# Performance work log

Hardware: AMD Instinct MI355X
Metric: run time of the kernel (lower is better)

## Reference

```python
import jax, jax.numpy as jnp
import numpy as np

B, S, D = 2, 1024, 1024
H, KV, HD = 16, 4, 64
E, F = 8, 3584
EPS = 1e-5
TOP_K = 2


def setup_inputs() -> dict:
    key = jax.random.key(0)
    ks = jax.random.split(key, 12)
    sc = 0.02
    inv_freq = 1.0 / (10000.0 ** (np.arange(0, HD, 2, dtype=np.float32) / HD))
    freqs = np.outer(np.arange(S, dtype=np.float32), inv_freq)
    emb = np.concatenate([freqs, freqs], axis=-1)  # [S, HD]
    return {
        'x': jax.random.normal(ks[0], (B, S, D), jnp.float32),
        'ln1_w': jnp.ones((D,), jnp.float32),
        'ln2_w': jnp.ones((D,), jnp.float32),
        'wq': jax.random.normal(ks[1], (H * HD, D), jnp.float32) * sc,
        'wk': jax.random.normal(ks[2], (KV * HD, D), jnp.float32) * sc,
        'wv': jax.random.normal(ks[3], (KV * HD, D), jnp.float32) * sc,
        'wo': jax.random.normal(ks[4], (D, H * HD), jnp.float32) * sc,
        'gate_w': jax.random.normal(ks[5], (E, D), jnp.float32) * sc,
        'w1': jax.random.normal(ks[6], (E, F, D), jnp.float32) * sc,
        'w2': jax.random.normal(ks[7], (E, D, F), jnp.float32) * sc,
        'w3': jax.random.normal(ks[8], (E, F, D), jnp.float32) * sc,
        'cos': jnp.asarray(np.cos(emb)),
        'sin': jnp.asarray(np.sin(emb)),
    }


def _rms_norm(x, w):
    var = jnp.mean(jnp.square(x), axis=-1, keepdims=True)
    return x * jax.lax.rsqrt(var + EPS) * w


def _rotate_half(x):
    x1, x2 = jnp.split(x, 2, axis=-1)
    return jnp.concatenate([-x2, x1], axis=-1)


def _attn(h, wq, wk, wv, wo, cos, sin):
    # h: [B,S,D]
    q = (h @ wq.T).reshape(B, S, H, HD).transpose(0, 2, 1, 3)      # [B,H,S,HD]
    k = (h @ wk.T).reshape(B, S, KV, HD).transpose(0, 2, 1, 3)     # [B,KV,S,HD]
    v = (h @ wv.T).reshape(B, S, KV, HD).transpose(0, 2, 1, 3)
    c = cos[None, None, :S, :]
    s = sin[None, None, :S, :]
    q = q * c + _rotate_half(q) * s
    k = k * c + _rotate_half(k) * s
    k = jnp.repeat(k, H // KV, axis=1)  # GQA expand -> [B,H,S,HD]
    v = jnp.repeat(v, H // KV, axis=1)
    scores = jnp.einsum('bhqd,bhkd->bhqk', q, k) / jnp.sqrt(jnp.float32(HD))
    causal = jnp.tril(jnp.ones((S, S), bool))
    scores = jnp.where(causal[None, None], scores, jnp.float32(-1e30))
    probs = jax.nn.softmax(scores, axis=-1)
    out = jnp.einsum('bhqk,bhkd->bhqd', probs, v)
    out = out.transpose(0, 2, 1, 3).reshape(B, S, H * HD)
    return out @ wo.T


def _moe(h, gate_w, w1, w2, w3):
    T = B * S
    hs = h.reshape(T, D)
    probs = jax.nn.softmax(hs @ gate_w.T, axis=-1)       # [T,E]
    _, sel = jax.lax.top_k(probs, TOP_K)                  # [T,2]
    rw = jnp.take_along_axis(probs, sel, axis=-1)
    rw = rw / jnp.sum(rw, axis=-1, keepdims=True)
    cw = jnp.zeros((T, E), hs.dtype).at[jnp.arange(T)[:, None], sel].add(rw)  # [T,E] combine weights
    h1 = jnp.einsum('td,efd->tef', hs, w1)               # [T,E,F]
    h3 = jnp.einsum('td,efd->tef', hs, w3)
    inter = jax.nn.silu(h1) * h3
    out = jnp.einsum('tef,edf,te->td', inter, w2, cw)
    return out.reshape(B, S, D)


def reference(x, ln1_w, ln2_w, wq, wk, wv, wo, gate_w, w1, w2, w3, cos, sin):
    h = x + _attn(_rms_norm(x, ln1_w), wq, wk, wv, wo, cos, sin)
    h = h + _moe(_rms_norm(h, ln2_w), gate_w, w1, w2, w3)
    return h
```

## Files before the change

kernel.cpp:

```cpp
#include <hip/hip_runtime.h>

typedef unsigned short u16;
using short8 = __attribute__((ext_vector_type(8))) short;
using f32x4  = __attribute__((ext_vector_type(4))) float;

#define TQ   2048
#define DM   1024
#define SLEN 1024
#define FDIM 3584
#define NEXP 8

static __device__ __forceinline__ u16 f2bf(float f) {
  union { float f; unsigned u; } a; a.f = f;
  unsigned r = a.u + 0x7fffu + ((a.u >> 16) & 1u);
  return (u16)(r >> 16);
}
static __device__ __forceinline__ float bf2f(u16 u) {
  union { unsigned u; float f; } a; a.u = ((unsigned)u) << 16;
  return a.f;
}
static __device__ __forceinline__ unsigned cvtpk(float lo, float hi) {
  unsigned r;
  asm volatile("v_cvt_pk_bf16_f32 %0, %1, %2" : "=v"(r) : "v"(lo), "v"(hi));
  return r;
}

static __device__ __forceinline__ void gload16(const void* g, void* l) {
  __builtin_amdgcn_global_load_lds((const __attribute__((address_space(1))) void*)g,
                                   (__attribute__((address_space(3))) void*)l, 16, 0, 0);
}

static __device__ __forceinline__ int xcd_lid(int bid, int cpx) {
  return (bid & 7) * cpx + (bid >> 3);
}

static __device__ __forceinline__ void cvtwr8(float4 a, float4 b, u16* dst) {
  uint4 u;
  u.x = cvtpk(a.x, a.y); u.y = cvtpk(a.z, a.w);
  u.z = cvtpk(b.x, b.y); u.w = cvtpk(b.z, b.w);
  *(uint4*)dst = u;
}

__global__ __launch_bounds__(256) void rmsnorm_kernel(
    const float* __restrict__ x, const float* __restrict__ w,
    u16* __restrict__ oh, u16* __restrict__ ol, float* __restrict__ of) {
  int t = blockIdx.x, tid = threadIdx.x;
  const float4* xr = (const float4*)(x + (size_t)t * DM);
  float4 v = xr[tid];
  float ss = v.x * v.x + v.y * v.y + v.z * v.z + v.w * v.w;
#pragma unroll
  for (int m = 1; m < 64; m <<= 1) ss += __shfl_xor(ss, m);
  __shared__ float red[4];
  if ((tid & 63) == 0) red[tid >> 6] = ss;
  __syncthreads();
  float tot = red[0] + red[1] + red[2] + red[3];
  float sc = rsqrtf(tot * (1.0f / DM) + 1e-5f);
  float4 wv = ((const float4*)w)[tid];
  float o0 = v.x * sc * wv.x, o1 = v.y * sc * wv.y, o2 = v.z * sc * wv.z, o3 = v.w * sc * wv.w;
  ushort4 hh;
  hh.x = f2bf(o0); hh.y = f2bf(o1); hh.z = f2bf(o2); hh.w = f2bf(o3);
  *(ushort4*)(oh + (size_t)t * DM + tid * 4) = hh;
  if (ol) {
    ushort4 ll;
    ll.x = f2bf(o0 - bf2f(hh.x)); ll.y = f2bf(o1 - bf2f(hh.y));
    ll.z = f2bf(o2 - bf2f(hh.z)); ll.w = f2bf(o3 - bf2f(hh.w));
    *(ushort4*)(ol + (size_t)t * DM + tid * 4) = ll;
  }
  if (of) {
    float4 o4; o4.x = o0; o4.y = o1; o4.z = o2; o4.w = o3;
    ((float4*)(of + (size_t)t * DM))[tid] = o4;
  }
}

__global__ __launch_bounds__(256) void wconv_split_kernel(
    const float* __restrict__ wq, const float* __restrict__ wk,
    const float* __restrict__ wv, const float* __restrict__ wo,
    u16* __restrict__ qkvh, u16* __restrict__ qkvl,
    u16* __restrict__ woh, u16* __restrict__ wol) {
  for (int i = blockIdx.x * 256 + threadIdx.x; i < 655360; i += 640 * 256) {
    int el = i * 4;
    const float* src; u16 *dh, *dl;
    if (el < 1572864) {
      int r = el >> 10, c = el & 1023;
      if (r < 1024) src = wq + el;
      else if (r < 1280) src = wk + (r - 1024) * 1024 + c;
      else src = wv + (r - 1280) * 1024 + c;
      dh = qkvh + el; dl = qkvl + el;
    } else {
      int e2 = el - 1572864;
      src = wo + e2; dh = woh + e2; dl = wol + e2;
    }
    float4 v = *(const float4*)src;
    ushort4 h, l;
    h.x = f2bf(v.x); h.y = f2bf(v.y); h.z = f2bf(v.z); h.w = f2bf(v.w);
    l.x = f2bf(v.x - bf2f(h.x)); l.y = f2bf(v.y - bf2f(h.y));
    l.z = f2bf(v.z - bf2f(h.z)); l.w = f2bf(v.w - bf2f(h.w));
    *(ushort4*)dh = h; *(ushort4*)dl = l;
  }
}

template <bool RESID>
__global__ __launch_bounds__(256) void gemm_split2_kernel(
    const u16* __restrict__ Ah, const u16* __restrict__ Al,
    const u16* __restrict__ Wh, const u16* __restrict__ Wl,
    float* __restrict__ C, const float* __restrict__ resid, int N, int cpx) {
  __shared__ u16 sAh[2][128][32], sAl[2][128][32], sWh[2][64][32], sWl[2][64][32];
  int lid = xcd_lid(blockIdx.x, cpx);
  int bm = lid & 15, bn = lid >> 4;
  int tid = threadIdx.x, lane = tid & 63, w = tid >> 6;
  int wm = w >> 1, wn = w & 1;
  int qi = lane & 15, g = lane >> 4;
  int lr = lane >> 2, lc = (lane & 3) * 8;
  const u16* pa0 = Ah + (size_t)(bm * 128 + w * 16 + lr) * DM + lc;
  const u16* pa1 = pa0 + 64 * DM;
  const u16* pl0 = Al + (size_t)(bm * 128 + w * 16 + lr) * DM + lc;
  const u16* pl1 = pl0 + 64 * DM;
  const u16* pw  = Wh + (size_t)(bn * 64 + w * 16 + lr) * DM + lc;
  const u16* pwl = Wl + (size_t)(bn * 64 + w * 16 + lr) * DM + lc;
  f32x4 acc[4][2] = {};
#define STG2(buf, kk) do { \
    gload16(pa0 + (kk), &sAh[buf][w * 16][0]); \
    gload16(pa1 + (kk), &sAh[buf][64 + w * 16][0]); \
    gload16(pl0 + (kk), &sAl[buf][w * 16][0]); \
    gload16(pl1 + (kk), &sAl[buf][64 + w * 16][0]); \
    gload16(pw  + (kk), &sWh[buf][w * 16][0]); \
    gload16(pwl + (kk), &sWl[buf][w * 16][0]); } while (0)
  STG2(0, 0);
  asm volatile("s_waitcnt vmcnt(0)" ::: "memory");
  __syncthreads();
  for (int ks = 0; ks < 32; ks++) {
    int cur = ks & 1;
    if (ks < 31) STG2(cur ^ 1, (ks + 1) * 32);
    short8 afh[4], afl[4], bfh[2], bfl[2];
#pragma unroll
    for (int i = 0; i < 4; i++) {
      afh[i] = *(short8*)&sAh[cur][wm * 64 + i * 16 + qi][g * 8];
      afl[i] = *(short8*)&sAl[cur][wm * 64 + i * 16 + qi][g * 8];
    }
#pragma unroll
    for (int i = 0; i < 2; i++) {
      bfh[i] = *(short8*)&sWh[cur][wn * 32 + i * 16 + qi][g * 8];
      bfl[i] = *(short8*)&sWl[cur][wn * 32 + i * 16 + qi][g * 8];
    }
#pragma unroll
    for (int mi = 0; mi < 4; mi++)
#pragma unroll
      for (int ni = 0; ni < 2; ni++) {
        f32x4 a = acc[mi][ni];
        a = __builtin_amdgcn_mfma_f32_16x16x32_bf16(afh[mi], bfh[ni], a, 0, 0, 0);
        a = __builtin_amdgcn_mfma_f32_16x16x32_bf16(afl[mi], bfh[ni], a, 0, 0, 0);
        a = __builtin_amdgcn_mfma_f32_16x16x32_bf16(afh[mi], bfl[ni], a, 0, 0, 0);
        acc[mi][ni] = a;
      }
    asm volatile("s_waitcnt vmcnt(0)" ::: "memory");
    __syncthreads();
  }
#undef STG2
#pragma unroll
  for (int mi = 0; mi < 4; mi++)
#pragma unroll
    for (int ni = 0; ni < 2; ni++) {
      int col = bn * 64 + wn * 32 + ni * 16 + qi;
#pragma unroll
      for (int r = 0; r < 4; r++) {
        int row = bm * 128 + wm * 64 + mi * 16 + g * 4 + r;
        float val = acc[mi][ni][r];
        if (RESID) val += resid[(size_t)row * N + col];
        C[(size_t)row * N + col] = val;
      }
    }
}

__global__ __launch_bounds__(256) void rope_split_kernel(
    const float* __restrict__ qkvf,
    const float* __restrict__ cosT, const float* __restrict__ sinT,
    u16* __restrict__ qh, u16* __restrict__ ql, u16* __restrict__ kh, u16* __restrict__ kl,
    u16* __restrict__ vh, u16* __restrict__ vl) {
  int t = blockIdx.x, tid = threadIdx.x;
  int s = t & (SLEN - 1);
  const float* rowp = qkvf + (size_t)t * 1536;
#pragma unroll
  for (int it = 0; it < 2; it++) {
    int i = it * 256 + tid;
    int hh = i >> 5, d = i & 31;
    float c = cosT[s * 64 + d], sn = sinT[s * 64 + d];
    size_t dst = (size_t)t * DM + hh * 64 + d;
    float x1 = rowp[hh * 64 + d], x2 = rowp[hh * 64 + d + 32];
    float o1 = x1 * c - x2 * sn;
    float o2 = x2 * c + x1 * sn;
    u16 h1 = f2bf(o1), h2 = f2bf(o2);
    qh[dst] = h1; qh[dst + 32] = h2;
    ql[dst] = f2bf(o1 - bf2f(h1)); ql[dst + 32] = f2bf(o2 - bf2f(h2));
  }
  if (tid < 128) {
    int hh = tid >> 5, d = tid & 31;
    float c = cosT[s * 64 + d], sn = sinT[s * 64 + d];
    size_t dst = (size_t)t * 256 + hh * 64 + d;
    float x1 = rowp[1024 + hh * 64 + d], x2 = rowp[1024 + hh * 64 + d + 32];
    float o1 = x1 * c - x2 * sn;
    float o2 = x2 * c + x1 * sn;
    u16 h1 = f2bf(o1), h2 = f2bf(o2);
    kh[dst] = h1; kh[dst + 32] = h2;
    kl[dst] = f2bf(o1 - bf2f(h1)); kl[dst + 32] = f2bf(o2 - bf2f(h2));
  }
  {
    size_t dst = (size_t)t * 256 + tid;
    float v = rowp[1280 + tid];
    u16 h = f2bf(v);
    vh[dst] = h; vl[dst] = f2bf(v - bf2f(h));
  }
}

__global__ __launch_bounds__(256) void attn_kernel(
    const u16* __restrict__ qh, const u16* __restrict__ ql,
    const u16* __restrict__ kh, const u16* __restrict__ kl,
    const u16* __restrict__ vh, const u16* __restrict__ vl,
    u16* __restrict__ oh, u16* __restrict__ ol) {
  __shared__ u16 sKh[64][72], sKl[64][72];
  __shared__ u16 sVh[64][72], sVl[64][72];
  __shared__ u16 sPh[4][16][72], sPl[4][16][72];
  int idx = blockIdx.x & 255;
  int p = idx & 7;
  int bh = idx >> 3;
  int b = bh >> 4, h = bh & 15, kvh = h >> 2;
  int qt = (blockIdx.x < 256) ? p : (15 - p);
  int tid = threadIdx.x, lane = tid & 63, w = tid >> 6;
  int qi = lane & 15, g = lane >> 4;
  int qrow = qt * 64 + w * 16 + qi;
  size_t qbase = ((size_t)(b * SLEN + qrow)) * DM + h * 64;
  short8 qfh[2], qfl[2];
#pragma unroll
  for (int ds = 0; ds < 2; ds++) {
    qfh[ds] = *(const short8*)(qh + qbase + ds * 32 + g * 8);
    qfl[ds] = *(const short8*)(ql + qbase + ds * 32 + g * 8);
  }
  f32x4 oacc[4] = {};
  float mrun = -1e30f, lrun = 0.f;
  int ktiles = qt + 1;
  for (int kt = 0; kt < ktiles; kt++) {
    __syncthreads();
    {
      int r = tid >> 3, cs = (tid & 7) * 8;
#pragma unroll
      for (int rr = 0; rr < 64; rr += 32) {
        int key = kt * 64 + rr + r;
        size_t src = ((size_t)(b * SLEN + key)) * 256 + kvh * 64 + cs;
        *(short8*)&sKh[rr + r][cs] = *(const short8*)(kh + src);
        *(short8*)&sKl[rr + r][cs] = *(const short8*)(kl + src);
        short8 vv = *(const short8*)(vh + src);
        short8 vv2 = *(const short8*)(vl + src);
#pragma unroll
        for (int j = 0; j < 8; j++) {
          sVh[cs + j][rr + r] = (u16)vv[j];
          sVl[cs + j][rr + r] = (u16)vv2[j];
        }
      }
    }
    __syncthreads();
    f32x4 sa[4];
#pragma unroll
    for (int kf = 0; kf < 4; kf++) {
      f32x4 a = {};
#pragma unroll
      for (int ds = 0; ds < 2; ds++) {
        short8 kfh = *(short8*)&sKh[kf * 16 + qi][ds * 32 + g * 8];
        short8 kfl = *(short8*)&sKl[kf * 16 + qi][ds * 32 + g * 8];
        a = __builtin_amdgcn_mfma_f32_16x16x32_bf16(kfh, qfh[ds], a, 0, 0, 0);
        a = __builtin_amdgcn_mfma_f32_16x16x32_bf16(kfl, qfh[ds], a, 0, 0, 0);
        a = __builtin_amdgcn_mfma_f32_16x16x32_bf16(kfh, qfl[ds], a, 0, 0, 0);
      }
      sa[kf] = a;
    }
    int qg = qt * 64 + w * 16 + qi;
    float sv[4][4];
    float tmax = -1e30f;
#pragma unroll
    for (int kf = 0; kf < 4; kf++)
#pragma unroll
      for (int r = 0; r < 4; r++) {
        int key = kt * 64 + kf * 16 + g * 4 + r;
        float s = sa[kf][r] * 0.125f;
        s = (key <= qg) ? s : -1e30f;
        sv[kf][r] = s;
        tmax = fmaxf(tmax, s);
      }
    tmax = fmaxf(tmax, __shfl_xor(tmax, 16));
    tmax = fmaxf(tmax, __shfl_xor(tmax, 32));
    float mn = fmaxf(mrun, tmax);
    float alpha = expf(mrun - mn);
    float psum = 0.f;
#pragma unroll
    for (int kf = 0; kf < 4; kf++) {
      float p0 = expf(sv[kf][0] - mn), p1 = expf(sv[kf][1] - mn);
      float p2 = expf(sv[kf][2] - mn), p3 = expf(sv[kf][3] - mn);
      psum += p0 + p1 + p2 + p3;
      ushort4 ph, pl;
      ph.x = f2bf(p0); ph.y = f2bf(p1); ph.z = f2bf(p2); ph.w = f2bf(p3);
      pl.x = f2bf(p0 - bf2f(ph.x)); pl.y = f2bf(p1 - bf2f(ph.y));
      pl.z = f2bf(p2 - bf2f(ph.z)); pl.w = f2bf(p3 - bf2f(ph.w));
      *(ushort4*)&sPh[w][qi][kf * 16 + g * 4] = ph;
      *(ushort4*)&sPl[w][qi][kf * 16 + g * 4] = pl;
    }
    psum += __shfl_xor(psum, 16);
    psum += __shfl_xor(psum, 32);
    lrun = lrun * alpha + psum;
    mrun = mn;
#pragma unroll
    for (int df = 0; df < 4; df++) {
      oacc[df][0] *= alpha; oacc[df][1] *= alpha;
      oacc[df][2] *= alpha; oacc[df][3] *= alpha;
    }
#pragma unroll
    for (int ks = 0; ks < 2; ks++) {
      short8 pfh = *(short8*)&sPh[w][qi][ks * 32 + g * 8];
      short8 pfl = *(short8*)&sPl[w][qi][ks * 32 + g * 8];
#pragma unroll
      for (int df = 0; df < 4; df++) {
        short8 vfh = *(short8*)&sVh[df * 16 + qi][ks * 32 + g * 8];
        short8 vfl = *(short8*)&sVl[df * 16 + qi][ks * 32 + g * 8];
        f32x4 a = oacc[df];
        a = __builtin_amdgcn_mfma_f32_16x16x32_bf16(vfh, pfh, a, 0, 0, 0);
        a = __builtin_amdgcn_mfma_f32_16x16x32_bf16(vfl, pfh, a, 0, 0, 0);
        a = __builtin_amdgcn_mfma_f32_16x16x32_bf16(vfh, pfl, a, 0, 0, 0);
        oacc[df] = a;
      }
    }
  }
  float inv = 1.0f / lrun;
  size_t obase = ((size_t)(b * SLEN + qt * 64 + w * 16 + qi)) * DM + h * 64;
#pragma unroll
  for (int df = 0; df < 4; df++) {
    float o0 = oacc[df][0] * inv, o1 = oacc[df][1] * inv;
    float o2 = oacc[df][2] * inv, o3 = oacc[df][3] * inv;
    ushort4 hh, ll;
    hh.x = f2bf(o0); hh.y = f2bf(o1); hh.z = f2bf(o2); hh.w = f2bf(o3);
    ll.x = f2bf(o0 - bf2f(hh.x)); ll.y = f2bf(o1 - bf2f(hh.y));
    ll.z = f2bf(o2 - bf2f(hh.z)); ll.w = f2bf(o3 - bf2f(hh.w));
    *(ushort4*)(oh + obase + df * 16 + g * 4) = hh;
    *(ushort4*)(ol + obase + df * 16 + g * 4) = ll;
  }
}

__global__ void zero8_kernel(int* p) { if (threadIdx.x < 8) p[threadIdx.x] = 0; }

__global__ __launch_bounds__(64) void gate_kernel(
    const float* __restrict__ hf, const float* __restrict__ gw,
    int* cnt, int* tok_e, int* tok_pos, float* tok_w) {
  int t = blockIdx.x, lane = threadIdx.x;
  float acc[8] = {0, 0, 0, 0, 0, 0, 0, 0};
  for (int i = lane; i < DM; i += 64) {
    float h = hf[(size_t)t * DM + i];
#pragma unroll
    for (int e = 0; e < 8; e++) acc[e] += h * gw[e * DM + i];
  }
#pragma unroll
  for (int e = 0; e < 8; e++)
#pragma unroll
    for (int m = 1; m < 64; m <<= 1) acc[e] += __shfl_xor(acc[e], m);
  if (lane == 0) {
    int i0 = 0;
#pragma unroll
    for (int e = 1; e < 8; e++) if (acc[e] > acc[i0]) i0 = e;
    int i1 = -1;
#pragma unroll
    for (int e = 0; e < 8; e++) if (e != i0 && (i1 < 0 || acc[e] > acc[i1])) i1 = e;
    float w0 = 1.0f;
    float w1 = expf(acc[i1] - acc[i0]);
    float rs = 1.0f / (w0 + w1);
    int p0 = atomicAdd(&cnt[i0], 1);
    int p1 = atomicAdd(&cnt[i1], 1);
    tok_e[t * 2] = i0; tok_e[t * 2 + 1] = i1;
    tok_pos[t * 2] = p0; tok_pos[t * 2 + 1] = p1;
    tok_w[t * 2] = w0 * rs; tok_w[t * 2 + 1] = w1 * rs;
  }
}

__global__ void schedule_kernel(const int* cnt, int* offs, int* mt,
                                int* row_e, int* row_bm) {
  if (threadIdx.x == 0) {
    int s = 0, m = 0;
    for (int e = 0; e < 8; e++) {
      offs[e] = s;
      int nb = (cnt[e] + 127) >> 7;
      for (int i = 0; i < nb; i++) { row_e[m] = e; row_bm[m] = i; m++; }
      s += cnt[e];
    }
    *mt = m;
  }
}

__global__ __launch_bounds__(256) void gather_kernel(
    const u16* __restrict__ hn2b, const int* __restrict__ tok_e,
    const int* __restrict__ tok_pos, const float* __restrict__ tok_w,
    const int* __restrict__ offs, u16* __restrict__ Xg,
    int* __restrict__ pair_tok, int* __restrict__ pair_slot, float* __restrict__ pair_w) {
  int t = blockIdx.x;
#pragma unroll
  for (int slot = 0; slot < 2; slot++) {
    int e = tok_e[t * 2 + slot];
    int p = offs[e] + tok_pos[t * 2 + slot];
    ((ushort4*)(Xg + (size_t)p * DM))[threadIdx.x] =
        ((const ushort4*)(hn2b + (size_t)t * DM))[threadIdx.x];
    if (threadIdx.x == 0) {
      pair_tok[p] = t; pair_slot[p] = slot; pair_w[p] = tok_w[t * 2 + slot];
    }
  }
}

__global__ __launch_bounds__(256) void moe_gemm13_kernel(
    const u16* __restrict__ Xg, const float* __restrict__ w1,
    const float* __restrict__ w3, const int* __restrict__ cnt,
    const int* __restrict__ offs, const int* __restrict__ mt,
    const int* __restrict__ row_e, const int* __restrict__ row_bm,
    u16* __restrict__ inter) {
  __shared__ u16 sA[3][128][32];
  __shared__ u16 sW1[3][64][32], sW3[3][64][32];
  int MT = *mt;
  int active = MT * 56;
  int cpx = (active + 7) >> 3;
  int xg8 = blockIdx.x >> 3;
  if (xg8 >= cpx) return;
  int lid = (blockIdx.x & 7) * cpx + xg8;
  if (lid >= active) return;
  int mrow = lid % MT, bn = lid / MT;
  int e = row_e[mrow], bm = row_bm[mrow];
  int count = cnt[e], off = offs[e];
  const u16* A = Xg + (size_t)off * DM;
  const float* W1 = w1 + (size_t)e * FDIM * DM;
  const float* W3 = w3 + (size_t)e * FDIM * DM;
  int tid = threadIdx.x, lane = tid & 63, w = tid >> 6;
  int wm = w >> 1, wn = w & 1;
  int qi = lane & 15, g = lane >> 4;
  int lrA = lane >> 2, lcA = (lane & 3) * 8;
  int ga0 = bm * 128 + w * 32 + lrA;      if (ga0 >= count) ga0 = count - 1;
  int ga1 = bm * 128 + w * 32 + 16 + lrA; if (ga1 >= count) ga1 = count - 1;
  const u16* pa0 = A + (size_t)ga0 * DM + lcA;
  const u16* pa1 = A + (size_t)ga1 * DM + lcA;
  int r16 = lane >> 2;
  int rW = w * 16 + r16;
  int cW = (lane & 3) * 8;
  const float* q1 = W1 + (size_t)(bn * 64 + rW) * DM + cW;
  const float* q3 = W3 + (size_t)(bn * 64 + rW) * DM + cW;
  int uW = ((lane & 3) ^ (r16 & 3)) * 8;
  f32x4 acc1[4][2] = {}, acc3[4][2] = {};
  float4 p1a = *(const float4*)q1, p1b = *(const float4*)(q1 + 4);
  float4 p3a = *(const float4*)q3, p3b = *(const float4*)(q3 + 4);
  float4 v1a = *(const float4*)(q1 + 32), v1b = *(const float4*)(q1 + 36);
  float4 v3a = *(const float4*)(q3 + 32), v3b = *(const float4*)(q3 + 36);
  __builtin_amdgcn_sched_barrier(0);
  gload16(pa0, &sA[0][w * 32][0]);
  gload16(pa1, &sA[0][w * 32 + 16][0]);
  gload16(pa0 + 32, &sA[1][w * 32][0]);
  gload16(pa1 + 32, &sA[1][w * 32 + 16][0]);
  asm volatile("s_waitcnt vmcnt(8)" ::: "memory");
  cvtwr8(p1a, p1b, &sW1[0][rW][uW]);
  cvtwr8(p3a, p3b, &sW3[0][rW][uW]);
  for (int ks = 0; ks < 32; ks++) {
    int cur = ks % 3;
    if (ks == 0)       asm volatile("s_waitcnt vmcnt(2) lgkmcnt(0)" ::: "memory");
    else if (ks == 31) asm volatile("s_waitcnt vmcnt(0) lgkmcnt(0)" ::: "memory");
    else               asm volatile("s_waitcnt vmcnt(6) lgkmcnt(0)" ::: "memory");
    __builtin_amdgcn_s_barrier();
    short8 af[4], b1[2], b3[2];
#pragma unroll
    for (int i = 0; i < 4; i++)
      af[i] = *(short8*)&sA[cur][wm * 64 + i * 16 + qi][g * 8];
#pragma unroll
    for (int ni = 0; ni < 2; ni++) {
      int rt = wn * 32 + ni * 16 + qi;
      int ui = (g ^ (rt & 3)) * 8;
      b1[ni] = *(short8*)&sW1[cur][rt][ui];
      b3[ni] = *(short8*)&sW3[cur][rt][ui];
    }
    __builtin_amdgcn_s_setprio(1);
#pragma unroll
    for (int mi = 0; mi < 4; mi++)
#pragma unroll
      for (int ni = 0; ni < 2; ni++) {
        acc1[mi][ni] = __builtin_amdgcn_mfma_f32_16x16x32_bf16(af[mi], b1[ni], acc1[mi][ni], 0, 0, 0);
        acc3[mi][ni] = __builtin_amdgcn_mfma_f32_16x16x32_bf16(af[mi], b3[ni], acc3[mi][ni], 0, 0, 0);
      }
    __builtin_amdgcn_s_setprio(0);
    if (ks < 31) {
      int nb = (ks + 1) % 3;
      cvtwr8(v1a, v1b, &sW1[nb][rW][uW]);
      cvtwr8(v3a, v3b, &sW3[nb][rW][uW]);
      if (ks < 30) {
        int k2 = (ks + 2) * 32;
        v1a = *(const float4*)(q1 + k2); v1b = *(const float4*)(q1 + k2 + 4);
        v3a = *(const float4*)(q3 + k2); v3b = *(const float4*)(q3 + k2 + 4);
        __builtin_amdgcn_sched_barrier(0);
        int ab = (ks + 2) % 3;
        gload16(pa0 + k2, &sA[ab][w * 32][0]);
        gload16(pa1 + k2, &sA[ab][w * 32 + 16][0]);
      }
    }
  }
#pragma unroll
  for (int mi = 0; mi < 4; mi++)
#pragma unroll
    for (int r = 0; r < 4; r++) {
      int row = bm * 128 + wm * 64 + mi * 16 + g * 4 + r;
      if (row < count) {
        size_t obase = (size_t)(off + row) * FDIM + bn * 64 + wn * 32;
#pragma unroll
        for (int ni = 0; ni < 2; ni++) {
          float c1 = acc1[mi][ni][r], c3 = acc3[mi][ni][r];
          float sv = c1 / (1.0f + expf(-c1)) * c3;
          inter[obase + ni * 16 + qi] = f2bf(sv);
        }
      }
    }
}

__global__ __launch_bounds__(256) void moe_gemm2_kernel(
    const u16* __restrict__ inter, const float* __restrict__ w2,
    const int* __restrict__ cnt, const int* __restrict__ offs,
    const int* __restrict__ mt, const int* __restrict__ row_e,
    const int* __restrict__ row_bm,
    const int* __restrict__ pair_tok, const int* __restrict__ pair_slot,
    const float* __restrict__ pair_w, float* __restrict__ pout) {
  __shared__ u16 sA[3][128][32];
  __shared__ u16 sW[3][64][32];
  int MT = *mt;
  int active = MT * 16;
  int cpx = (active + 7) >> 3;
  int xg8 = blockIdx.x >> 3;
  if (xg8 >= cpx) return;
  int lid = (blockIdx.x & 7) * cpx + xg8;
  if (lid >= active) return;
  int mrow = lid % MT, bn = lid / MT;
  int e = row_e[mrow], bm = row_bm[mrow];
  int count = cnt[e], off = offs[e];
  const u16* A = inter + (size_t)off * FDIM;
  const float* W = w2 + (size_t)e * DM * FDIM;
  int tid = threadIdx.x, lane = tid & 63, w = tid >> 6;
  int wm = w >> 1, wn = w & 1;
  int qi = lane & 15, g = lane >> 4;
  int lrA = lane >> 2, lcA = (lane & 3) * 8;
  int ga0 = bm * 128 + w * 32 + lrA;      if (ga0 >= count) ga0 = count - 1;
  int ga1 = bm * 128 + w * 32 + 16 + lrA; if (ga1 >= count) ga1 = count - 1;
  const u16* pa0 = A + (size_t)ga0 * FDIM + lcA;
  const u16* pa1 = A + (size_t)ga1 * FDIM + lcA;
  int r16 = lane >> 2;
  int rW = w * 16 + r16;
  int cW = (lane & 3) * 8;
  const float* qw = W + (size_t)(bn * 64 + rW) * FDIM + cW;
  int uW = ((lane & 3) ^ (r16 & 3)) * 8;
  f32x4 acc[4][2] = {};
  const int NK = FDIM / 32;
  float4 ta = *(const float4*)qw, tb = *(const float4*)(qw + 4);
  float4 va = *(const float4*)(qw + 32), vb = *(const float4*)(qw + 36);
  __builtin_amdgcn_sched_barrier(0);
  gload16(pa0, &sA[0][w * 32][0]);
  gload16(pa1, &sA[0][w * 32 + 16][0]);
  gload16(pa0 + 32, &sA[1][w * 32][0]);
  gload16(pa1 + 32, &sA[1][w * 32 + 16][0]);
  asm volatile("s_waitcnt vmcnt(6)" ::: "memory");
  cvtwr8(ta, tb, &sW[0][rW][uW]);
  for (int ks = 0; ks < NK; ks++) {
    int cur = ks % 3;
    if (ks == 0)           asm volatile("s_waitcnt vmcnt(2) lgkmcnt(0)" ::: "memory");
    else if (ks == NK - 1) asm volatile("s_waitcnt vmcnt(0) lgkmcnt(0)" ::: "memory");
    else                   asm volatile("s_waitcnt vmcnt(4) lgkmcnt(0)" ::: "memory");
    __builtin_amdgcn_s_barrier();
    short8 af[4], bfr[2];
#pragma unroll
    for (int i = 0; i < 4; i++)
      af[i] = *(short8*)&sA[cur][wm * 64 + i * 16 + qi][g * 8];
#pragma unroll
    for (int ni = 0; ni < 2; ni++) {
      int rt = wn * 32 + ni * 16 + qi;
      bfr[ni] = *(short8*)&sW[cur][rt][(g ^ (rt & 3)) * 8];
    }
    __builtin_amdgcn_s_setprio(1);
#pragma unroll
    for (int mi = 0; mi < 4; mi++)
#pragma unroll
      for (int ni = 0; ni < 2; ni++)
        acc[mi][ni] = __builtin_amdgcn_mfma_f32_16x16x32_bf16(af[mi], bfr[ni], acc[mi][ni], 0, 0, 0);
    __builtin_amdgcn_s_setprio(0);
    if (ks < NK - 1) {
      int nb = (ks + 1) % 3;
      cvtwr8(va, vb, &sW[nb][rW][uW]);
      if (ks < NK - 2) {
        int k2 = (ks + 2) * 32;
        va = *(const float4*)(qw + k2); vb = *(const float4*)(qw + k2 + 4);
        __builtin_amdgcn_sched_barrier(0);
        int ab = (ks + 2) % 3;
        gload16(pa0 + k2, &sA[ab][w * 32][0]);
        gload16(pa1 + k2, &sA[ab][w * 32 + 16][0]);
      }
    }
  }
#pragma unroll
  for (int mi = 0; mi < 4; mi++)
#pragma unroll
    for (int r = 0; r < 4; r++) {
      int row = bm * 128 + wm * 64 + mi * 16 + g * 4 + r;
      if (row < count) {
        int p = off + row;
        int t = pair_tok[p];
        float wgt = pair_w[p];
        size_t obase = ((size_t)pair_slot[p] * TQ + t) * DM + bn * 64 + wn * 32;
#pragma unroll
        for (int ni = 0; ni < 2; ni++)
          pout[obase + ni * 16 + qi] = acc[mi][ni][r] * wgt;
      }
    }
}

__global__ __launch_bounds__(256) void combine_kernel(
    const float* __restrict__ h, const float* __restrict__ pout, float* __restrict__ out) {
  size_t i = (size_t)blockIdx.x * 256 + threadIdx.x;
  float4 a = ((const float4*)h)[i];
  float4 b0 = ((const float4*)pout)[i];
  float4 b1 = ((const float4*)pout)[i + (size_t)TQ * DM / 4];
  float4 r;
  r.x = a.x + b0.x + b1.x; r.y = a.y + b0.y + b1.y;
  r.z = a.z + b0.z + b1.z; r.w = a.w + b0.w + b1.w;
  ((float4*)out)[i] = r;
}

extern "C" void kernel_launch(void* const* d_in, const int* in_sizes, int n_in,
                              void* d_out, int out_size, void* d_ws, size_t ws_size,
                              hipStream_t stream) {
  (void)in_sizes; (void)n_in; (void)out_size; (void)ws_size;
  const float* x    = (const float*)d_in[0];
  const float* ln1  = (const float*)d_in[1];
  const float* ln2  = (const float*)d_in[2];
  const float* wq   = (const float*)d_in[3];
  const float* wk   = (const float*)d_in[4];
  const float* wv   = (const float*)d_in[5];
  const float* wo   = (const float*)d_in[6];
  const float* gw   = (const float*)d_in[7];
  const float* w1   = (const float*)d_in[8];
  const float* w2   = (const float*)d_in[9];
  const float* w3   = (const float*)d_in[10];
  const float* cosT = (const float*)d_in[11];
  const float* sinT = (const float*)d_in[12];

  char* mb = (char*)d_ws;
  const size_t MB = 1024 * 1024;
  u16*   qhb  = (u16*)(mb + 0 * MB);
  u16*   qlb  = (u16*)(mb + 4 * MB);
  u16*   khb  = (u16*)(mb + 8 * MB);
  u16*   klb  = (u16*)(mb + 9 * MB);
  u16*   vhb  = (u16*)(mb + 10 * MB);
  u16*   vlb  = (u16*)(mb + 11 * MB);
  u16*   hn2b = (u16*)(mb + 0 * MB);
  float* hn2f = (float*)(mb + 4 * MB);
  u16*   ahb  = (u16*)(mb + 12 * MB);
  u16*   alb  = (u16*)(mb + 16 * MB);
  u16*   Xg   = (u16*)(mb + 12 * MB);
  u16*   hn1h = (u16*)(mb + 20 * MB);
  u16*   hn1l = (u16*)(mb + 24 * MB);
  u16*   inter= (u16*)(mb + 20 * MB);
  float* qkvf = (float*)(mb + 28 * MB);
  float* h_res= (float*)(mb + 48 * MB);
  u16*   woh  = (u16*)(mb + 56 * MB);
  u16*   wol  = (u16*)(mb + 58 * MB);
  float* pout = (float*)(mb + 56 * MB);
  u16*   wqkvh= (u16*)(mb + 60 * MB);
  u16*   wqkvl= (u16*)(mb + 63 * MB);
  int*   cnt  = (int*)(mb + 72 * MB);
  int*   offs = cnt + 8;
  int*   mtp  = cnt + 16;
  int*   row_e  = cnt + 17;
  int*   row_bm = cnt + 57;
  int*   tok_e  = cnt + 128;
  int*   tok_pos = tok_e + 4096;
  float* tok_w   = (float*)(tok_pos + 4096);
  int*   pair_tok  = (int*)(tok_w + 4096);
  int*   pair_slot = pair_tok + 4096;
  float* pair_w    = (float*)(pair_slot + 4096);

  wconv_split_kernel<<<640, 256, 0, stream>>>(wq, wk, wv, wo, wqkvh, wqkvl, woh, wol);
  rmsnorm_kernel<<<TQ, 256, 0, stream>>>(x, ln1, hn1h, hn1l, nullptr);
  gemm_split2_kernel<false><<<384, 256, 0, stream>>>(hn1h, hn1l, wqkvh, wqkvl, qkvf, nullptr, 1536, 48);
  rope_split_kernel<<<TQ, 256, 0, stream>>>(qkvf, cosT, sinT, qhb, qlb, khb, klb, vhb, vlb);
  attn_kernel<<<512, 256, 0, stream>>>(qhb, qlb, khb, klb, vhb, vlb, ahb, alb);
  gemm_split2_kernel<true><<<256, 256, 0, stream>>>(ahb, alb, woh, wol, h_res, x, 1024, 32);
  rmsnorm_kernel<<<TQ, 256, 0, stream>>>(h_res, ln2, hn2b, nullptr, hn2f);
  zero8_kernel<<<1, 64, 0, stream>>>(cnt);
  gate_kernel<<<TQ, 64, 0, stream>>>(hn2f, gw, cnt, tok_e, tok_pos, tok_w);
  schedule_kernel<<<1, 64, 0, stream>>>(cnt, offs, mtp, row_e, row_bm);
  gather_kernel<<<TQ, 256, 0, stream>>>(hn2b, tok_e, tok_pos, tok_w, offs, Xg,
                                        pair_tok, pair_slot, pair_w);
  moe_gemm13_kernel<<<2240, 256, 0, stream>>>(Xg, w1, w3, cnt, offs, mtp,
                                              row_e, row_bm, inter);
  moe_gemm2_kernel<<<640, 256, 0, stream>>>(inter, w2, cnt, offs, mtp,
                                            row_e, row_bm,
                                            pair_tok, pair_slot, pair_w, pout);
  combine_kernel<<<TQ, 256, 0, stream>>>(h_res, pout, (float*)d_out);
}
```

Measured before the change: 472.2 us.

## Fuse pre-norm with weight conversion, fuse rmsnorm with gate, triple-buffer split GEMM

Merges the weight bf16 hi/lo conversion and the first RMSNorm into one launch, and fuses the second RMSNorm with the MoE gate logits and top-2 routing so the fp32 normalized copy is no longer written and reread. The dense split-bf16 GEMM moves from double to triple buffering, with one barrier per k-step, partial vmcnt waits and raised MFMA priority so loads overlap compute. This cuts launches and memory traffic. The three-stage LDS use lowers occupancy, and the gate now reads from a 256-thread block.

```diff
diff --git a/kernel.cpp b/kernel.cpp
--- a/kernel.cpp
+++ b/kernel.cpp
@@ -41,43 +41,40 @@
   *(uint4*)dst = u;
 }
 
-__global__ __launch_bounds__(256) void rmsnorm_kernel(
-    const float* __restrict__ x, const float* __restrict__ w,
-    u16* __restrict__ oh, u16* __restrict__ ol, float* __restrict__ of) {
-  int t = blockIdx.x, tid = threadIdx.x;
-  const float4* xr = (const float4*)(x + (size_t)t * DM);
-  float4 v = xr[tid];
-  float ss = v.x * v.x + v.y * v.y + v.z * v.z + v.w * v.w;
-#pragma unroll
-  for (int m = 1; m < 64; m <<= 1) ss += __shfl_xor(ss, m);
-  __shared__ float red[4];
-  if ((tid & 63) == 0) red[tid >> 6] = ss;
-  __syncthreads();
-  float tot = red[0] + red[1] + red[2] + red[3];
-  float sc = rsqrtf(tot * (1.0f / DM) + 1e-5f);
-  float4 wv = ((const float4*)w)[tid];
-  float o0 = v.x * sc * wv.x, o1 = v.y * sc * wv.y, o2 = v.z * sc * wv.z, o3 = v.w * sc * wv.w;
-  ushort4 hh;
-  hh.x = f2bf(o0); hh.y = f2bf(o1); hh.z = f2bf(o2); hh.w = f2bf(o3);
-  *(ushort4*)(oh + (size_t)t * DM + tid * 4) = hh;
-  if (ol) {
+__global__ __launch_bounds__(256) void fused_pre_kernel(
+    const float* __restrict__ x, const float* __restrict__ ln1,
+    u16* __restrict__ oh, u16* __restrict__ ol,
+    const float* __restrict__ wq, const float* __restrict__ wk,
+    const float* __restrict__ wv, const float* __restrict__ wo,
+    u16* __restrict__ qkvh, u16* __restrict__ qkvl,
+    u16* __restrict__ woh, u16* __restrict__ wol) {
+  int tid = threadIdx.x;
+  if (blockIdx.x < 2048) {
+    int t = blockIdx.x;
+    const float4* xr = (const float4*)(x + (size_t)t * DM);
+    float4 v = xr[tid];
+    float ss = v.x * v.x + v.y * v.y + v.z * v.z + v.w * v.w;
+#pragma unroll
+    for (int m = 1; m < 64; m <<= 1) ss += __shfl_xor(ss, m);
+    __shared__ float red[4];
+    if ((tid & 63) == 0) red[tid >> 6] = ss;
+    __syncthreads();
+    float tot = red[0] + red[1] + red[2] + red[3];
+    float sc = rsqrtf(tot * (1.0f / DM) + 1e-5f);
+    float4 wv_ = ((const float4*)ln1)[tid];
+    float o0 = v.x * sc * wv_.x, o1 = v.y * sc * wv_.y;
+    float o2 = v.z * sc * wv_.z, o3 = v.w * sc * wv_.w;
+    ushort4 hh;
+    hh.x = f2bf(o0); hh.y = f2bf(o1); hh.z = f2bf(o2); hh.w = f2bf(o3);
+    *(ushort4*)(oh + (size_t)t * DM + tid * 4) = hh;
     ushort4 ll;
     ll.x = f2bf(o0 - bf2f(hh.x)); ll.y = f2bf(o1 - bf2f(hh.y));
     ll.z = f2bf(o2 - bf2f(hh.z)); ll.w = f2bf(o3 - bf2f(hh.w));
     *(ushort4*)(ol + (size_t)t * DM + tid * 4) = ll;
-  }
-  if (of) {
-    float4 o4; o4.x = o0; o4.y = o1; o4.z = o2; o4.w = o3;
-    ((float4*)(of + (size_t)t * DM))[tid] = o4;
-  }
-}
-
-__global__ __launch_bounds__(256) void wconv_split_kernel(
-    const float* __restrict__ wq, const float* __restrict__ wk,
-    const float* __restrict__ wv, const float* __restrict__ wo,
-    u16* __restrict__ qkvh, u16* __restrict__ qkvl,
-    u16* __restrict__ woh, u16* __restrict__ wol) {
-  for (int i = blockIdx.x * 256 + threadIdx.x; i < 655360; i += 640 * 256) {
+    return;
+  }
+  int wb = blockIdx.x - 2048;
+  for (int i = wb * 256 + tid; i < 655360; i += 640 * 256) {
     int el = i * 4;
     const float* src; u16 *dh, *dl;
     if (el < 1572864) {
@@ -99,12 +96,70 @@
   }
 }
 
+__global__ __launch_bounds__(256) void rmsnorm_gate_kernel(
+    const float* __restrict__ x, const float* __restrict__ w,
+    const float* __restrict__ gw, u16* __restrict__ oh,
+    int* cnt, int* tok_e, int* tok_pos, float* tok_w) {
+  int t = blockIdx.x, tid = threadIdx.x;
+  float4 v = ((const float4*)(x + (size_t)t * DM))[tid];
+  float ss = v.x * v.x + v.y * v.y + v.z * v.z + v.w * v.w;
+#pragma unroll
+  for (int m = 1; m < 64; m <<= 1) ss += __shfl_xor(ss, m);
+  __shared__ float red[4];
+  __shared__ float gred[4][8];
+  if ((tid & 63) == 0) red[tid >> 6] = ss;
+  __syncthreads();
+  float tot = red[0] + red[1] + red[2] + red[3];
+  float sc = rsqrtf(tot * (1.0f / DM) + 1e-5f);
+  float4 wv_ = ((const float4*)w)[tid];
+  float o0 = v.x * sc * wv_.x, o1 = v.y * sc * wv_.y;
+  float o2 = v.z * sc * wv_.z, o3 = v.w * sc * wv_.w;
+  ushort4 hh;
+  hh.x = f2bf(o0); hh.y = f2bf(o1); hh.z = f2bf(o2); hh.w = f2bf(o3);
+  *(ushort4*)(oh + (size_t)t * DM + tid * 4) = hh;
+  float acc[8];
+#pragma unroll
+  for (int e = 0; e < 8; e++) {
+    float4 ge = ((const float4*)(gw + e * DM))[tid];
+    acc[e] = o0 * ge.x + o1 * ge.y + o2 * ge.z + o3 * ge.w;
+  }
+#pragma unroll
+  for (int e = 0; e < 8; e++)
+#pragma unroll
+    for (int m = 1; m < 64; m <<= 1) acc[e] += __shfl_xor(acc[e], m);
+  int lane = tid & 63, wvi = tid >> 6;
+  if (lane == 0)
+#pragma unroll
+    for (int e = 0; e < 8; e++) gred[wvi][e] = acc[e];
+  __syncthreads();
+  if (tid == 0) {
+    float l[8];
+#pragma unroll
+    for (int e = 0; e < 8; e++)
+      l[e] = gred[0][e] + gred[1][e] + gred[2][e] + gred[3][e];
+    int i0 = 0;
+#pragma unroll
+    for (int e = 1; e < 8; e++) if (l[e] > l[i0]) i0 = e;
+    int i1 = -1;
+#pragma unroll
+    for (int e = 0; e < 8; e++) if (e != i0 && (i1 < 0 || l[e] > l[i1])) i1 = e;
+    float w0 = 1.0f;
+    float w1 = expf(l[i1] - l[i0]);
+    float rs = 1.0f / (w0 + w1);
+    int p0 = atomicAdd(&cnt[i0], 1);
+    int p1 = atomicAdd(&cnt[i1], 1);
+    tok_e[t * 2] = i0; tok_e[t * 2 + 1] = i1;
+    tok_pos[t * 2] = p0; tok_pos[t * 2 + 1] = p1;
+    tok_w[t * 2] = w0 * rs; tok_w[t * 2 + 1] = w1 * rs;
+  }
+}
+
 template <bool RESID>
-__global__ __launch_bounds__(256) void gemm_split2_kernel(
+__global__ __launch_bounds__(256) void gemm_split3_kernel(
     const u16* __restrict__ Ah, const u16* __restrict__ Al,
     const u16* __restrict__ Wh, const u16* __restrict__ Wl,
     float* __restrict__ C, const float* __restrict__ resid, int N, int cpx) {
-  __shared__ u16 sAh[2][128][32], sAl[2][128][32], sWh[2][64][32], sWl[2][64][32];
+  __shared__ u16 sAh[3][128][32], sAl[3][128][32], sWh[3][64][32], sWl[3][64][32];
   int lid = xcd_lid(blockIdx.x, cpx);
   int bm = lid & 15, bn = lid >> 4;
   int tid = threadIdx.x, lane = tid & 63, w = tid >> 6;
@@ -118,19 +173,20 @@
   const u16* pw  = Wh + (size_t)(bn * 64 + w * 16 + lr) * DM + lc;
   const u16* pwl = Wl + (size_t)(bn * 64 + w * 16 + lr) * DM + lc;
   f32x4 acc[4][2] = {};
-#define STG2(buf, kk) do { \
+#define STG3(buf, kk) do { \
     gload16(pa0 + (kk), &sAh[buf][w * 16][0]); \
     gload16(pa1 + (kk), &sAh[buf][64 + w * 16][0]); \
     gload16(pl0 + (kk), &sAl[buf][w * 16][0]); \
     gload16(pl1 + (kk), &sAl[buf][64 + w * 16][0]); \
     gload16(pw  + (kk), &sWh[buf][w * 16][0]); \
     gload16(pwl + (kk), &sWl[buf][w * 16][0]); } while (0)
-  STG2(0, 0);
-  asm volatile("s_waitcnt vmcnt(0)" ::: "memory");
-  __syncthreads();
+  STG3(0, 0);
+  STG3(1, 32);
   for (int ks = 0; ks < 32; ks++) {
-    int cur = ks & 1;
-    if (ks < 31) STG2(cur ^ 1, (ks + 1) * 32);
+    int cur = ks % 3;
+    if (ks == 31) asm volatile("s_waitcnt vmcnt(0) lgkmcnt(0)" ::: "memory");
+    else          asm volatile("s_waitcnt vmcnt(6) lgkmcnt(0)" ::: "memory");
+    __builtin_amdgcn_s_barrier();
     short8 afh[4], afl[4], bfh[2], bfl[2];
 #pragma unroll
     for (int i = 0; i < 4; i++) {
@@ -142,6 +198,7 @@
       bfh[i] = *(short8*)&sWh[cur][wn * 32 + i * 16 + qi][g * 8];
       bfl[i] = *(short8*)&sWl[cur][wn * 32 + i * 16 + qi][g * 8];
     }
+    __builtin_amdgcn_s_setprio(1);
 #pragma unroll
     for (int mi = 0; mi < 4; mi++)
 #pragma unroll
@@ -152,10 +209,10 @@
         a = __builtin_amdgcn_mfma_f32_16x16x32_bf16(afh[mi], bfl[ni], a, 0, 0, 0);
         acc[mi][ni] = a;
       }
-    asm volatile("s_waitcnt vmcnt(0)" ::: "memory");
-    __syncthreads();
-  }
-#undef STG2
+    __builtin_amdgcn_s_setprio(0);
+    if (ks < 30) STG3((ks + 2) % 3, (ks + 2) * 32);
+  }
+#undef STG3
 #pragma unroll
   for (int mi = 0; mi < 4; mi++)
 #pragma unroll
@@ -342,38 +399,6 @@
 }
 
 __global__ void zero8_kernel(int* p) { if (threadIdx.x < 8) p[threadIdx.x] = 0; }
-
-__global__ __launch_bounds__(64) void gate_kernel(
-    const float* __restrict__ hf, const float* __restrict__ gw,
-    int* cnt, int* tok_e, int* tok_pos, float* tok_w) {
-  int t = blockIdx.x, lane = threadIdx.x;
-  float acc[8] = {0, 0, 0, 0, 0, 0, 0, 0};
-  for (int i = lane; i < DM; i += 64) {
-    float h = hf[(size_t)t * DM + i];
-#pragma unroll
-    for (int e = 0; e < 8; e++) acc[e] += h * gw[e * DM + i];
-  }
-#pragma unroll
-  for (int e = 0; e < 8; e++)
-#pragma unroll
-    for (int m = 1; m < 64; m <<= 1) acc[e] += __shfl_xor(acc[e], m);
-  if (lane == 0) {
-    int i0 = 0;
-#pragma unroll
-    for (int e = 1; e < 8; e++) if (acc[e] > acc[i0]) i0 = e;
-    int i1 = -1;
-#pragma unroll
-    for (int e = 0; e < 8; e++) if (e != i0 && (i1 < 0 || acc[e] > acc[i1])) i1 = e;
-    float w0 = 1.0f;
-    float w1 = expf(acc[i1] - acc[i0]);
-    float rs = 1.0f / (w0 + w1);
-    int p0 = atomicAdd(&cnt[i0], 1);
-    int p1 = atomicAdd(&cnt[i1], 1);
-    tok_e[t * 2] = i0; tok_e[t * 2 + 1] = i1;
-    tok_pos[t * 2] = p0; tok_pos[t * 2 + 1] = p1;
-    tok_w[t * 2] = w0 * rs; tok_w[t * 2 + 1] = w1 * rs;
-  }
-}
 
 __global__ void schedule_kernel(const int* cnt, int* offs, int* mt,
                                 int* row_e, int* row_bm) {
@@ -649,7 +674,6 @@
   u16*   vhb  = (u16*)(mb + 10 * MB);
   u16*   vlb  = (u16*)(mb + 11 * MB);
   u16*   hn2b = (u16*)(mb + 0 * MB);
-  float* hn2f = (float*)(mb + 4 * MB);
   u16*   ahb  = (u16*)(mb + 12 * MB);
   u16*   alb  = (u16*)(mb + 16 * MB);
   u16*   Xg   = (u16*)(mb + 12 * MB);
@@ -675,15 +699,16 @@
   int*   pair_slot = pair_tok + 4096;
   float* pair_w    = (float*)(pair_slot + 4096);
 
-  wconv_split_kernel<<<640, 256, 0, stream>>>(wq, wk, wv, wo, wqkvh, wqkvl, woh, wol);
-  rmsnorm_kernel<<<TQ, 256, 0, stream>>>(x, ln1, hn1h, hn1l, nullptr);
-  gemm_split2_kernel<false><<<384, 256, 0, stream>>>(hn1h, hn1l, wqkvh, wqkvl, qkvf, nullptr, 1536, 48);
+  fused_pre_kernel<<<2688, 256, 0, stream>>>(x, ln1, hn1h, hn1l,
+                                             wq, wk, wv, wo,
+                                             wqkvh, wqkvl, woh, wol);
+  gemm_split3_kernel<false><<<384, 256, 0, stream>>>(hn1h, hn1l, wqkvh, wqkvl, qkvf, nullptr, 1536, 48);
   rope_split_kernel<<<TQ, 256, 0, stream>>>(qkvf, cosT, sinT, qhb, qlb, khb, klb, vhb, vlb);
   attn_kernel<<<512, 256, 0, stream>>>(qhb, qlb, khb, klb, vhb, vlb, ahb, alb);
-  gemm_split2_kernel<true><<<256, 256, 0, stream>>>(ahb, alb, woh, wol, h_res, x, 1024, 32);
-  rmsnorm_kernel<<<TQ, 256, 0, stream>>>(h_res, ln2, hn2b, nullptr, hn2f);
+  gemm_split3_kernel<true><<<256, 256, 0, stream>>>(ahb, alb, woh, wol, h_res, x, 1024, 32);
   zero8_kernel<<<1, 64, 0, stream>>>(cnt);
-  gate_kernel<<<TQ, 64, 0, stream>>>(hn2f, gw, cnt, tok_e, tok_pos, tok_w);
+  rmsnorm_gate_kernel<<<TQ, 256, 0, stream>>>(h_res, ln2, gw, hn2b,
+                                              cnt, tok_e, tok_pos, tok_w);
   schedule_kernel<<<1, 64, 0, stream>>>(cnt, offs, mtp, row_e, row_bm);
   gather_kernel<<<TQ, 256, 0, stream>>>(hn2b, tok_e, tok_pos, tok_w, offs, Xg,
                                         pair_tok, pair_slot, pair_w);
```

Result: faster. 436.8 us (-7.5%).
